# Kernel tuning notes

Measured on AMD Instinct MI355X. Metric: run time of the kernel, lower is better.

Reference implementation:

```python
import jax, jax.numpy as jnp
import numpy as np

N_HEAD, D_HEAD = 10, 38
D_MODEL, D_INNER = 380, 900
QLEN, BSZ = 1024, 4
MIN_LEN, MAX_LEN = -1024, 1024
EPS = 1e-5
SCALE = 1.0 / D_HEAD ** 0.5


def _ln(x, g, b):
    m = x.mean(-1, keepdims=True)
    v = ((x - m) ** 2).mean(-1, keepdims=True)
    return (x - m) / jnp.sqrt(v + EPS) * g + b


def setup_inputs() -> dict:
    key = jax.random.key(0)
    ks = jax.random.split(key, 10)
    s = 0.02
    w = jax.random.normal(ks[0], (QLEN, BSZ, D_MODEL), jnp.float32)
    # sinusoidal relative position embeddings over positions max_len .. min_len
    pos = jnp.arange(MAX_LEN, MIN_LEN - 1, -1, dtype=jnp.float32)  # [rlen]
    inv_freq = 1.0 / (10000.0 ** (jnp.arange(0, D_MODEL, 2, dtype=jnp.float32) / D_MODEL))
    sin_inp = pos[:, None] * inv_freq[None, :]
    r = jnp.concatenate([jnp.sin(sin_inp), jnp.cos(sin_inp)], axis=-1)  # [rlen, d_model]
    # causal mask, True = attend; layout [qlen, klen, bsz]
    attn_mask = jnp.broadcast_to(jnp.tril(jnp.ones((QLEN, QLEN), bool))[:, :, None], (QLEN, QLEN, BSZ))
    attn_relpos = jax.random.randint(ks[1], (BSZ, QLEN, QLEN), MIN_LEN, MAX_LEN + 1).astype(jnp.int32)
    return {
        'w': w,
        'r': r,
        'r_w_bias': s * jax.random.normal(ks[2], (N_HEAD, D_HEAD), jnp.float32),
        'r_r_bias': s * jax.random.normal(ks[3], (N_HEAD, D_HEAD), jnp.float32),
        'qkv_w': s * jax.random.normal(ks[4], (3 * N_HEAD * D_HEAD, D_MODEL), jnp.float32),
        'r_w': s * jax.random.normal(ks[5], (N_HEAD * D_HEAD, D_MODEL), jnp.float32),
        'o_w': s * jax.random.normal(ks[6], (D_MODEL, N_HEAD * D_HEAD), jnp.float32),
        'ln1_g': jnp.ones(D_MODEL, jnp.float32), 'ln1_b': jnp.zeros(D_MODEL, jnp.float32),
        'ff_w1': s * jax.random.normal(ks[7], (D_INNER, D_MODEL), jnp.float32),
        'ff_b1': jnp.zeros(D_INNER, jnp.float32),
        'ff_w2': s * jax.random.normal(ks[8], (D_MODEL, D_INNER), jnp.float32),
        'ff_b2': jnp.zeros(D_MODEL, jnp.float32),
        'ln2_g': jnp.ones(D_MODEL, jnp.float32), 'ln2_b': jnp.zeros(D_MODEL, jnp.float32),
        'attn_mask': attn_mask,
        'attn_relpos': attn_relpos,
        'min_len': MIN_LEN,
        'max_len': MAX_LEN,
    }


def reference(w, r, r_w_bias, r_r_bias, qkv_w, r_w, o_w, ln1_g, ln1_b,
              ff_w1, ff_b1, ff_w2, ff_b2, ln2_g, ln2_b,
              attn_mask, attn_relpos, min_len, max_len):
    qlen, bsz, _ = w.shape
    # qkv projection (no mems, post-lnorm)
    heads = jnp.einsum('ibm,hm->ibh', w, qkv_w)  # [q, b, 3*nh*dh]
    q, k, v = jnp.split(heads, 3, axis=-1)
    q = q.reshape(qlen, bsz, N_HEAD, D_HEAD)
    k = k.reshape(qlen, bsz, N_HEAD, D_HEAD)
    v = v.reshape(qlen, bsz, N_HEAD, D_HEAD)
    rk = (r @ r_w.T).reshape(-1, N_HEAD, D_HEAD)  # [rlen, nh, dh]
    # content score AC and position score BD (Transformer-XL)
    AC = jnp.einsum('ibnd,jbnd->ijbn', q + r_w_bias, k)   # [q, k, b, n]
    BD = jnp.einsum('ibnd,jnd->ijbn', q + r_r_bias, rk)   # [q, rlen, b, n]
    # gather-based relative position indexing (attn_relpos path)
    idx = (max_len - jnp.clip(attn_relpos, min_len, max_len)).transpose(1, 2, 0)  # [q, k, b]
    idx4 = jnp.broadcast_to(idx[..., None], idx.shape + (N_HEAD,))
    BD = jnp.take_along_axis(BD, idx4, axis=1)            # [q, k, b, n]
    score = (AC + BD) * SCALE
    score = jnp.where(attn_mask[:, :, :, None], score, -jnp.inf)
    prob = jax.nn.softmax(score, axis=1)
    vec = jnp.einsum('ijbn,jbnd->ibnd', prob, v).reshape(qlen, bsz, N_HEAD * D_HEAD)
    attn_out = vec @ o_w.T
    out = _ln(w + attn_out, ln1_g, ln1_b)
    # position-wise FF, post-lnorm
    core = jax.nn.relu(out @ ff_w1.T + ff_b1) @ ff_w2.T + ff_b2
    return _ln(out + core, ln2_g, ln2_b)
```

## Files before the change

kernel.cpp:

```cpp
#include <hip/hip_runtime.h>
#include <math.h>

#define QLEN 1024
#define BSZ 4
#define NH 10
#define DH 38
#define DM 380
#define DI 900
#define H3 1140
#define RLEN 2049
#define RLP 2112
#define SCALE 0.16222142113076254f
#define KS 2

typedef unsigned short ushortt;
typedef __attribute__((ext_vector_type(8))) short short8;
typedef __attribute__((ext_vector_type(4))) float float4v;

__device__ __forceinline__ float bf2f(ushortt u) {
    return __uint_as_float(((unsigned int)u) << 16);
}
__device__ __forceinline__ ushortt f2bf(float f) {
    unsigned int u = __float_as_uint(f);
    u += 0x7fffu + ((u >> 16) & 1u);
    return (ushortt)(u >> 16);
}

__global__ __launch_bounds__(256)
void convpad(const float* __restrict__ src, ushortt* __restrict__ dst,
             int R, int C, int Rp, int Cp) {
    const int total = Rp * Cp;
    for (int i = blockIdx.x * 256 + threadIdx.x; i < total; i += gridDim.x * 256) {
        int r = i / Cp, c = i - r * Cp;
        float v = (r < R && c < C) ? src[(size_t)r * C + c] : 0.f;
        dst[i] = f2bf(v);
    }
}

__global__ __launch_bounds__(256)
void init_pads(float* __restrict__ qwp, float* __restrict__ Kp, float* __restrict__ Vp,
               ushortt* __restrict__ vec) {
    const int i = blockIdx.x * 256 + threadIdx.x;
    if (i < BSZ * NH * 1024 * 2) {
        size_t idx = (size_t)(i >> 1) * 40 + 38 + (i & 1);
        qwp[idx] = 0.f; Kp[idx] = 0.f; Vp[idx] = 0.f;
    }
    if (i < 4096 * 4) {
        vec[(size_t)(i >> 2) * 384 + 380 + (i & 3)] = 0;
    }
}

template<int EPI>
__global__ __launch_bounds__(256)
void gemm_mfma(const ushortt* __restrict__ A, const ushortt* __restrict__ B,
               const float* __restrict__ bias, void* __restrict__ Cout,
               int M, int N, int Kpp, int ldc,
               const float* __restrict__ bias2, float* __restrict__ out2,
               float* __restrict__ out3, float* __restrict__ out4) {
    __shared__ __align__(16) ushortt As[128 * 32];
    __shared__ __align__(16) ushortt Bs[64 * 32];
    const int tid = threadIdx.x;
    const int wid = tid >> 6, lane = tid & 63;
    const int bRow = blockIdx.y * 128, bCol = blockIdx.x * 64;

    float4v acc[2][4];
    const float4v zz = {0.f, 0.f, 0.f, 0.f};
    #pragma unroll
    for (int m = 0; m < 2; ++m)
        #pragma unroll
        for (int n = 0; n < 4; ++n) acc[m][n] = zz;

    const int arow = tid >> 1, acol = (tid & 1) * 16;
    const int brow = tid >> 2, bcol = (tid & 3) * 8;
    const int fr = lane & 15, kg = lane >> 4;

    for (int k0 = 0; k0 < Kpp; k0 += 32) {
        const ushortt* ag = A + (size_t)(bRow + arow) * Kpp + k0 + acol;
        float4v a0 = *(const float4v*)ag;
        float4v a1 = *(const float4v*)(ag + 8);
        const ushortt* bg = B + (size_t)(bCol + brow) * Kpp + k0 + bcol;
        float4v b0 = *(const float4v*)bg;
        __syncthreads();
        *(float4v*)&As[arow * 32 + acol] = a0;
        *(float4v*)&As[arow * 32 + acol + 8] = a1;
        *(float4v*)&Bs[brow * 32 + bcol] = b0;
        __syncthreads();

        short8 bf[4];
        #pragma unroll
        for (int n = 0; n < 4; ++n)
            bf[n] = *(const short8*)&Bs[(n * 16 + fr) * 32 + kg * 8];
        #pragma unroll
        for (int m = 0; m < 2; ++m) {
            short8 af = *(const short8*)&As[(wid * 32 + m * 16 + fr) * 32 + kg * 8];
            #pragma unroll
            for (int n = 0; n < 4; ++n)
                acc[m][n] = __builtin_amdgcn_mfma_f32_16x16x32_bf16(af, bf[n], acc[m][n], 0, 0, 0);
        }
    }

    #pragma unroll
    for (int m = 0; m < 2; ++m)
        #pragma unroll
        for (int n = 0; n < 4; ++n)
            #pragma unroll
            for (int j = 0; j < 4; ++j) {
                const int row = bRow + wid * 32 + m * 16 + (lane >> 4) * 4 + j;
                const int col = bCol + n * 16 + (lane & 15);
                const float v = acc[m][n][j];
                if (EPI == 0) {
                    if (row < M && col < N) ((float*)Cout)[(size_t)row * ldc + col] = v;
                } else if (EPI == 3) {
                    if (row < M && col < 928) {
                        float h = (col < DI) ? fmaxf(v + bias[col], 0.f) : 0.f;
                        ((ushortt*)Cout)[(size_t)row * 928 + col] = f2bf(h);
                    }
                } else if (EPI == 4) {
                    if (row < M && col < N) ((float*)Cout)[(size_t)row * ldc + col] = v + bias[col];
                } else if (EPI == 5) {
                    if (col < H3) {
                        int part = col / 380;
                        int c = col - part * 380;
                        int nh = c / 38, d = c - nh * 38;
                        int q = row >> 2, b2 = row & 3;
                        size_t idx = (((size_t)b2 * NH + nh) * 1024 + q) * 40 + d;
                        if (part == 0) {
                            ((float*)Cout)[idx] = v + bias[c];
                            ((ushortt*)out2)[(((size_t)b2 * NH + nh) * 1024 + q) * 64 + d]
                                = f2bf(v + bias2[c]);
                        } else if (part == 1) out3[idx] = v;
                        else out4[idx] = v;
                    }
                } else {
                    if (row < RLEN && col < DM) {
                        int nh = col / 38, d = col - nh * 38;
                        ((ushortt*)Cout)[((size_t)nh * RLP + row) * 64 + d] = f2bf(v);
                    }
                }
            }
}

__global__ __launch_bounds__(256)
void bd_gemm(const ushortt* __restrict__ qr, const ushortt* __restrict__ rk,
             ushortt* __restrict__ BD, int bofs) {
    __shared__ __align__(16) ushortt As[64][72];
    __shared__ __align__(16) ushortt Bs[32][72];
    __shared__ __align__(16) ushortt Call[64 * 32 * 10];
    const int tid = threadIdx.x;
    const int wid = tid >> 6, lane = tid & 63;
    const int jt = blockIdx.x, qt = blockIdx.y, lb = blockIdx.z;
    const int j0 = jt * 32, q0 = qt * 64;
    const int fr = lane & 15, kg = lane >> 4;
    const int jcount = min(32, RLEN - j0);

    for (int n = 0; n < NH; ++n) {
        const ushortt* Ab = qr + (((size_t)(bofs + lb) * NH + n) * 1024 + q0) * 64;
        const ushortt* Bb = rk + ((size_t)n * RLP + j0) * 64;
        __syncthreads();
        {
            int rr = tid >> 2, cc = (tid & 3) * 16;
            *(float4v*)&As[rr][cc] = *(const float4v*)(Ab + (size_t)rr * 64 + cc);
            *(float4v*)&As[rr][cc + 8] = *(const float4v*)(Ab + (size_t)rr * 64 + cc + 8);
            int br = tid >> 3, bc = (tid & 7) * 8;
            *(float4v*)&Bs[br][bc] = *(const float4v*)(Bb + (size_t)br * 64 + bc);
        }
        __syncthreads();
        float4v acc[2] = {{0.f,0.f,0.f,0.f},{0.f,0.f,0.f,0.f}};
        #pragma unroll
        for (int ks = 0; ks < 64; ks += 32) {
            short8 af = *(const short8*)&As[wid * 16 + fr][ks + kg * 8];
            #pragma unroll
            for (int c = 0; c < 2; ++c) {
                short8 bfr = *(const short8*)&Bs[c * 16 + fr][ks + kg * 8];
                acc[c] = __builtin_amdgcn_mfma_f32_16x16x32_bf16(af, bfr, acc[c], 0, 0, 0);
            }
        }
        #pragma unroll
        for (int c = 0; c < 2; ++c)
            #pragma unroll
            for (int jj = 0; jj < 4; ++jj) {
                int rq = wid * 16 + (lane >> 4) * 4 + jj;
                int cj = c * 16 + (lane & 15);
                Call[(rq * 32 + cj) * 10 + n] = f2bf(acc[c][jj]);
            }
    }
    __syncthreads();
    const int rowdw = jcount * 5;
    const unsigned* Cdw = (const unsigned*)Call;
    unsigned* G = (unsigned*)BD;
    for (int idx = tid; idx < 64 * rowdw; idx += 256) {
        int rr = idx / rowdw, rem = idx - rr * rowdw;
        size_t gdw = ((((size_t)lb * 1024 + q0 + rr) * RLEN + j0) * 10) / 2 + rem;
        G[gdw] = Cdw[rr * 160 + rem];
    }
}

__global__ __launch_bounds__(256)
void attn4(const float* __restrict__ qwp, const float* __restrict__ Kp,
           const float* __restrict__ Vp, const ushortt* __restrict__ BD,
           const int* __restrict__ relpos,
           float* __restrict__ op, float2* __restrict__ ml, int b0, int nb) {
    const int bid = blockIdx.x;
    const int xcd = bid & 7, t = bid >> 3;
    const int gl = t / 20, member = t - gl * 20;
    const int G = gl * 8 + xcd;
    const int qc = 31 - G / nb;
    const int lbd = G - (31 - qc) * nb;
    const int n = member % NH, s = member / NH;
    const int qbase = qc * 32;
    const int b = b0 + lbd;
    const int tid = threadIdx.x;
    const int row = tid >> 3, kg = tid & 7;
    const int qi = qbase + row;
    const size_t bn = (size_t)b * NH + n;
    const size_t prow = ((size_t)s * (BSZ * NH) + bn) * 1024 + qi;

    const int ntchunk = (qbase + 95) >> 6;
    const int tbeg = s * 8;
    const int tend = min(tbeg + 8, ntchunk);
    if (tbeg >= tend) {
        if (kg == 0) ml[prow] = make_float2(-INFINITY, 0.f);
        return;
    }

    __shared__ __align__(16) float KtL[64 * 40];
    __shared__ __align__(16) float VtL[64 * 40];
    __shared__ float pL[32 * 66];

    const float* Kbase = Kp + bn * 1024 * 40;
    const float* Vbase = Vp + bn * 1024 * 40;

    float4v qw[10];
    {
        const float4v* src = (const float4v*)(qwp + (bn * 1024 + qi) * 40);
        #pragma unroll
        for (int i = 0; i < 10; ++i) qw[i] = src[i];
    }
    float o[5] = {0.f, 0.f, 0.f, 0.f, 0.f};
    float mrun = -INFINITY, lrun = 0.f;
    const int* rp = relpos + ((size_t)b * QLEN + qi) * QLEN;
    const ushortt* bdrow = BD + (((size_t)lbd * 1024 + qi) * RLEN) * NH + n;

    int jv[8]; float bdv[8];
    {
        const int k0 = tbeg * 64;
        #pragma unroll
        for (int ss = 0; ss < 8; ++ss) {
            const int kk = k0 + kg + ss * 8;
            int j = -1;
            if (kk <= qi) {
                int rpv = rp[kk];
                rpv = rpv < -1024 ? -1024 : (rpv > 1024 ? 1024 : rpv);
                j = 1024 - rpv;
            }
            jv[ss] = j;
        }
        #pragma unroll
        for (int ss = 0; ss < 8; ++ss)
            bdv[ss] = (jv[ss] >= 0) ? bf2f(bdrow[(size_t)jv[ss] * NH]) : 0.f;
    }

    for (int kt = tbeg; kt < tend; ++kt) {
        const int k0 = kt * 64;
        __syncthreads();
        {
            const float4v* ks = (const float4v*)(Kbase + (size_t)k0 * 40);
            const float4v* vs = (const float4v*)(Vbase + (size_t)k0 * 40);
            for (int e = tid; e < 640; e += 256) {
                ((float4v*)KtL)[e] = ks[e];
                ((float4v*)VtL)[e] = vs[e];
            }
        }
        __syncthreads();

        float sarr[8];
        float pmax = -INFINITY;
        #pragma unroll
        for (int ss = 0; ss < 8; ++ss) {
            float sv = -INFINITY;
            if (jv[ss] >= 0) {
                const int k = kg + ss * 8;
                float acc1 = 0.f;
                const float4v* kt4 = (const float4v*)(KtL + k * 40);
                #pragma unroll
                for (int i = 0; i < 10; ++i) {
                    float4v kv = kt4[i];
                    acc1 += qw[i][0] * kv[0] + qw[i][1] * kv[1]
                          + qw[i][2] * kv[2] + qw[i][3] * kv[3];
                }
                sv = (acc1 + bdv[ss]) * SCALE;
            }
            sarr[ss] = sv;
            pmax = fmaxf(pmax, sv);
        }
        pmax = fmaxf(pmax, __shfl_xor(pmax, 1, 64));
        pmax = fmaxf(pmax, __shfl_xor(pmax, 2, 64));
        pmax = fmaxf(pmax, __shfl_xor(pmax, 4, 64));
        const float nm = fmaxf(mrun, pmax);
        const float corr = __expf(mrun - nm);
        float psum = 0.f;
        float* prw = pL + row * 66;
        #pragma unroll
        for (int ss = 0; ss < 8; ++ss) {
            float p = __expf(sarr[ss] - nm);
            psum += p;
            prw[kg + ss * 8] = p;
        }
        psum += __shfl_xor(psum, 1, 64);
        psum += __shfl_xor(psum, 2, 64);
        psum += __shfl_xor(psum, 4, 64);
        lrun = lrun * corr + psum;
        mrun = nm;
        #pragma unroll
        for (int jj = 0; jj < 5; ++jj) o[jj] *= corr;

        int jn[8]; float bdn[8];
        if (kt + 1 < tend) {
            const int k0n = (kt + 1) * 64;
            #pragma unroll
            for (int ss = 0; ss < 8; ++ss) {
                const int kk = k0n + kg + ss * 8;
                int j = -1;
                if (kk <= qi) {
                    int rpv = rp[kk];
                    rpv = rpv < -1024 ? -1024 : (rpv > 1024 ? 1024 : rpv);
                    j = 1024 - rpv;
                }
                jn[ss] = j;
            }
            #pragma unroll
            for (int ss = 0; ss < 8; ++ss)
                bdn[ss] = (jn[ss] >= 0) ? bf2f(bdrow[(size_t)jn[ss] * NH]) : 0.f;
        } else {
            #pragma unroll
            for (int ss = 0; ss < 8; ++ss) { jn[ss] = -1; bdn[ss] = 0.f; }
        }

        int kmax = qi - k0 + 1; if (kmax > 64) kmax = 64;
        #pragma unroll 4
        for (int k = 0; k < kmax; ++k) {
            float p = prw[k];
            const float* vr = VtL + k * 40;
            float4v v4 = *(const float4v*)(vr + 4 * kg);
            float v1 = vr[32 + kg];
            o[0] += p * v4[0]; o[1] += p * v4[1];
            o[2] += p * v4[2]; o[3] += p * v4[3];
            o[4] += p * v1;
        }
        #pragma unroll
        for (int ss = 0; ss < 8; ++ss) { jv[ss] = jn[ss]; bdv[ss] = bdn[ss]; }
    }
    float* oprow = op + prow * 40;
    #pragma unroll
    for (int jj = 0; jj < 4; ++jj) oprow[4 * kg + jj] = o[jj];
    oprow[32 + kg] = o[4];
    if (kg == 0) ml[prow] = make_float2(mrun, lrun);
}

__global__ __launch_bounds__(256)
void attn_combine(const float* __restrict__ op, const float2* __restrict__ ml,
                  ushortt* __restrict__ vec) {
    const int idx = blockIdx.x * 256 + threadIdx.x;
    if (idx >= BSZ * NH * 1024 * 38) return;
    const int d = idx % 38;
    const int rh = idx / 38;
    const int q = rh & 1023;
    const int bn = rh >> 10;
    const int b = bn / NH, n = bn - b * NH;
    const float2 a = ml[rh];
    const float2 c = ml[(size_t)BSZ * NH * 1024 + rh];
    const float M = fmaxf(a.x, c.x);
    float l = 0.f, o = 0.f;
    if (a.y > 0.f) {
        float w = __expf(a.x - M);
        l += a.y * w;
        o += op[(size_t)rh * 40 + d] * w;
    }
    if (c.y > 0.f) {
        float w = __expf(c.x - M);
        l += c.y * w;
        o += op[((size_t)BSZ * NH * 1024 + rh) * 40 + d] * w;
    }
    vec[((size_t)q * BSZ + b) * 384 + (size_t)n * 38 + d] = f2bf(o / l);
}

template<bool WRITE_BF>
__global__ __launch_bounds__(256)
void ln_kernel(const float* __restrict__ x1, const float* __restrict__ x2,
               const float* __restrict__ g, const float* __restrict__ bb,
               float* __restrict__ outf, ushortt* __restrict__ outbf) {
    const int row = blockIdx.x;
    const float* p1 = x1 + (size_t)row * DM;
    const float* p2 = x2 + (size_t)row * DM;
    __shared__ float xb[DM];
    __shared__ float red[256];
    const int tid = threadIdx.x;
    float s = 0.f;
    for (int i = tid; i < DM; i += 256) { float v = p1[i] + p2[i]; xb[i] = v; s += v; }
    red[tid] = s; __syncthreads();
    for (int st = 128; st > 0; st >>= 1) { if (tid < st) red[tid] += red[tid + st]; __syncthreads(); }
    const float mean = red[0] / DM;
    __syncthreads();
    float s2 = 0.f;
    for (int i = tid; i < DM; i += 256) { float d = xb[i] - mean; s2 += d * d; }
    red[tid] = s2; __syncthreads();
    for (int st = 128; st > 0; st >>= 1) { if (tid < st) red[tid] += red[tid + st]; __syncthreads(); }
    const float rstd = rsqrtf(red[0] / DM + 1e-5f);
    for (int i = tid; i < (WRITE_BF ? 384 : DM); i += 256) {
        float v = 0.f;
        if (i < DM) {
            v = (xb[i] - mean) * rstd * g[i] + bb[i];
            outf[(size_t)row * DM + i] = v;
        }
        if (WRITE_BF) outbf[(size_t)row * 384 + i] = f2bf(i < DM ? v : 0.f);
    }
}

extern "C" void kernel_launch(void* const* d_in, const int* in_sizes, int n_in,
                              void* d_out, int out_size, void* d_ws, size_t ws_size,
                              hipStream_t stream) {
    const float* w     = (const float*)d_in[0];
    const float* r     = (const float*)d_in[1];
    const float* rwb   = (const float*)d_in[2];
    const float* rrb   = (const float*)d_in[3];
    const float* qkv_w = (const float*)d_in[4];
    const float* r_w   = (const float*)d_in[5];
    const float* o_w   = (const float*)d_in[6];
    const float* ln1g  = (const float*)d_in[7];
    const float* ln1b  = (const float*)d_in[8];
    const float* ffw1  = (const float*)d_in[9];
    const float* ffb1  = (const float*)d_in[10];
    const float* ffw2  = (const float*)d_in[11];
    const float* ffb2  = (const float*)d_in[12];
    const float* ln2g  = (const float*)d_in[13];
    const float* ln2b  = (const float*)d_in[14];
    const int*   relpos = (const int*)d_in[16];
    float* out = (float*)d_out;

    char* cur = (char*)d_ws;
    auto alloc = [&](size_t bytes) { char* p = cur; cur += (bytes + 255) & ~(size_t)255; return p; };
    ushortt* w_bf    = (ushortt*)alloc((size_t)4096 * 384 * 2);
    ushortt* qkv_bf  = (ushortt*)alloc((size_t)1152 * 384 * 2);
    ushortt* r_bf    = (ushortt*)alloc((size_t)2176 * 384 * 2);
    ushortt* rw_bf   = (ushortt*)alloc((size_t)384 * 384 * 2);
    ushortt* ow_bf   = (ushortt*)alloc((size_t)384 * 384 * 2);
    ushortt* f1_bf   = (ushortt*)alloc((size_t)960 * 384 * 2);
    ushortt* f2_bf   = (ushortt*)alloc((size_t)384 * 928 * 2);
    float*   qwp     = (float*)alloc((size_t)BSZ * NH * 1024 * 40 * 4);
    float*   Kpp     = (float*)alloc((size_t)BSZ * NH * 1024 * 40 * 4);
    float*   Vpp     = (float*)alloc((size_t)BSZ * NH * 1024 * 40 * 4);
    ushortt* qr_bf   = (ushortt*)alloc((size_t)BSZ * NH * 1024 * 64 * 2);
    ushortt* rk_bf   = (ushortt*)alloc((size_t)NH * RLP * 64 * 2);
    ushortt* vec_bf  = (ushortt*)alloc((size_t)4096 * 384 * 2);
    ushortt* out1_bf = (ushortt*)alloc((size_t)4096 * 384 * 2);
    ushortt* h1_bf   = (ushortt*)alloc((size_t)4096 * 928 * 2);
    float*   attnf   = (float*)alloc((size_t)4096 * DM * 4);
    float*   out1f   = (float*)alloc((size_t)4096 * DM * 4);
    float*   core    = (float*)alloc((size_t)4096 * DM * 4);

    float*  op_part = attnf;
    float2* ml_part = (float2*)(attnf + (size_t)KS * BSZ * NH * 1024 * 40);

    const size_t bd_b_bytes = (size_t)1024 * RLEN * NH * 2;
    ushortt* BD = (ushortt*)alloc(bd_b_bytes * BSZ);
    bool full = ((size_t)(cur - (char*)d_ws) <= ws_size);
    if (!full) { cur = (char*)BD; BD = (ushortt*)alloc(bd_b_bytes); }

    auto cgrid = [](size_t total) { return dim3((unsigned)((total + 255) / 256)); };
    hipMemsetAsync(qr_bf, 0, (size_t)BSZ * NH * 1024 * 64 * 2, stream);
    hipMemsetAsync(rk_bf, 0, (size_t)NH * RLP * 64 * 2, stream);
    convpad<<<cgrid((size_t)4096 * 384), 256, 0, stream>>>(w, w_bf, 4096, DM, 4096, 384);
    convpad<<<cgrid((size_t)1152 * 384), 256, 0, stream>>>(qkv_w, qkv_bf, H3, DM, 1152, 384);
    convpad<<<cgrid((size_t)2176 * 384), 256, 0, stream>>>(r, r_bf, RLEN, DM, 2176, 384);
    convpad<<<cgrid((size_t)384 * 384), 256, 0, stream>>>(r_w, rw_bf, DM, DM, 384, 384);
    convpad<<<cgrid((size_t)384 * 384), 256, 0, stream>>>(o_w, ow_bf, DM, DM, 384, 384);
    convpad<<<cgrid((size_t)960 * 384), 256, 0, stream>>>(ffw1, f1_bf, DI, DM, 960, 384);
    convpad<<<cgrid((size_t)384 * 928), 256, 0, stream>>>(ffw2, f2_bf, DM, DI, 384, 928);
    init_pads<<<cgrid((size_t)BSZ * NH * 1024 * 2), 256, 0, stream>>>(qwp, Kpp, Vpp, vec_bf);

    gemm_mfma<5><<<dim3(18, 32), 256, 0, stream>>>(w_bf, qkv_bf, rwb, qwp, 4096, H3, 384, 0,
                                                   rrb, (float*)qr_bf, Kpp, Vpp);
    gemm_mfma<6><<<dim3(6, 17), 256, 0, stream>>>(r_bf, rw_bf, nullptr, rk_bf, RLEN, DM, 384, 0,
                                                  nullptr, nullptr, nullptr, nullptr);
    if (full) {
        bd_gemm<<<dim3(65, 16, BSZ), 256, 0, stream>>>(qr_bf, rk_bf, BD, 0);
        attn4<<<dim3(2560), 256, 0, stream>>>(qwp, Kpp, Vpp, BD, relpos,
                                              op_part, ml_part, 0, BSZ);
    } else {
        for (int b = 0; b < BSZ; ++b) {
            bd_gemm<<<dim3(65, 16, 1), 256, 0, stream>>>(qr_bf, rk_bf, BD, b);
            attn4<<<dim3(640), 256, 0, stream>>>(qwp, Kpp, Vpp, BD, relpos,
                                                 op_part, ml_part, b, 1);
        }
    }
    attn_combine<<<cgrid((size_t)BSZ * NH * 1024 * 38), 256, 0, stream>>>(op_part, ml_part, vec_bf);
    gemm_mfma<0><<<dim3(6, 32), 256, 0, stream>>>(vec_bf, ow_bf, nullptr, attnf, 4096, DM, 384, DM,
                                                  nullptr, nullptr, nullptr, nullptr);
    ln_kernel<true><<<4096, 256, 0, stream>>>(w, attnf, ln1g, ln1b, out1f, out1_bf);
    gemm_mfma<3><<<dim3(15, 32), 256, 0, stream>>>(out1_bf, f1_bf, ffb1, h1_bf, 4096, DI, 384, 928,
                                                   nullptr, nullptr, nullptr, nullptr);
    gemm_mfma<4><<<dim3(6, 32), 256, 0, stream>>>(h1_bf, f2_bf, ffb2, core, 4096, DM, 928, DM,
                                                  nullptr, nullptr, nullptr, nullptr);
    ln_kernel<false><<<4096, 256, 0, stream>>>(out1f, core, ln2g, ln2b, out, nullptr);
}
```

Before: 405.9 us.

## Split attention key range into up to four chunks, store K/V and partials in bf16

The attention kernel now splits each query chunk's key range into chunks of four 64-key tiles, giving up to four splits instead of two. A new block-index mapping assigns blocks only to splits that have work, and the grid grows from 2560 to 3200 blocks. K and V are written by the QKV GEMM as bf16 and converted to fp32 when loaded into shared memory, which halves their global traffic. Partial outputs are also stored as bf16, and the combine kernel merges a variable number of splits. In exchange, the software prefetch of relpos/BD for the next tile is dropped, and bf16 K/V and partials lose some precision.

After: 402.4 us. About the same (-0.8%).

```diff
diff --git a/kernel.cpp b/kernel.cpp
--- a/kernel.cpp
+++ b/kernel.cpp
@@ -11,7 +11,6 @@
 #define RLEN 2049
 #define RLP 2112
 #define SCALE 0.16222142113076254f
-#define KS 2
 
 typedef unsigned short ushortt;
 typedef __attribute__((ext_vector_type(8))) short short8;
@@ -38,12 +37,12 @@
 }
 
 __global__ __launch_bounds__(256)
-void init_pads(float* __restrict__ qwp, float* __restrict__ Kp, float* __restrict__ Vp,
+void init_pads(float* __restrict__ qwp, ushortt* __restrict__ Kb, ushortt* __restrict__ Vb,
                ushortt* __restrict__ vec) {
     const int i = blockIdx.x * 256 + threadIdx.x;
     if (i < BSZ * NH * 1024 * 2) {
         size_t idx = (size_t)(i >> 1) * 40 + 38 + (i & 1);
-        qwp[idx] = 0.f; Kp[idx] = 0.f; Vp[idx] = 0.f;
+        qwp[idx] = 0.f; Kb[idx] = 0; Vb[idx] = 0;
     }
     if (i < 4096 * 4) {
         vec[(size_t)(i >> 2) * 384 + 380 + (i & 3)] = 0;
@@ -128,8 +127,8 @@
                             ((float*)Cout)[idx] = v + bias[c];
                             ((ushortt*)out2)[(((size_t)b2 * NH + nh) * 1024 + q) * 64 + d]
                                 = f2bf(v + bias2[c]);
-                        } else if (part == 1) out3[idx] = v;
-                        else out4[idx] = v;
+                        } else if (part == 1) ((ushortt*)out3)[idx] = f2bf(v);
+                        else ((ushortt*)out4)[idx] = f2bf(v);
                     }
                 } else {
                     if (row < RLEN && col < DM) {
@@ -196,39 +195,40 @@
 }
 
 __global__ __launch_bounds__(256)
-void attn4(const float* __restrict__ qwp, const float* __restrict__ Kp,
-           const float* __restrict__ Vp, const ushortt* __restrict__ BD,
+void attn5(const float* __restrict__ qwp, const ushortt* __restrict__ Kp,
+           const ushortt* __restrict__ Vp, const ushortt* __restrict__ BD,
            const int* __restrict__ relpos,
-           float* __restrict__ op, float2* __restrict__ ml, int b0, int nb) {
+           ushortt* __restrict__ op, float2* __restrict__ ml, int b0, int nb) {
     const int bid = blockIdx.x;
     const int xcd = bid & 7, t = bid >> 3;
-    const int gl = t / 20, member = t - gl * 20;
+    const int gl = t / 10, n = t - gl * 10;
     const int G = gl * 8 + xcd;
-    const int qc = 31 - G / nb;
-    const int lbd = G - (31 - qc) * nb;
-    const int n = member % NH, s = member / NH;
+    int qc, lb, s;
+    {
+        const int c3 = 32 * nb, c2 = 24 * nb, c1 = 16 * nb;
+        if (G < c3)                { qc = 31 - G / (4 * nb); int r2 = G % (4 * nb); lb = r2 >> 2; s = r2 & 3; }
+        else if (G < c3 + c2)      { int l2 = G - c3; qc = 23 - l2 / (3 * nb); int r2 = l2 % (3 * nb); lb = r2 / 3; s = r2 % 3; }
+        else if (G < c3 + c2 + c1) { int l2 = G - c3 - c2; qc = 15 - l2 / (2 * nb); int r2 = l2 % (2 * nb); lb = r2 >> 1; s = r2 & 1; }
+        else                       { int l2 = G - c3 - c2 - c1; qc = 7 - l2 / nb; lb = l2 % nb; s = 0; }
+    }
     const int qbase = qc * 32;
-    const int b = b0 + lbd;
+    const int b = b0 + lb;
     const int tid = threadIdx.x;
     const int row = tid >> 3, kg = tid & 7;
     const int qi = qbase + row;
     const size_t bn = (size_t)b * NH + n;
     const size_t prow = ((size_t)s * (BSZ * NH) + bn) * 1024 + qi;
 
-    const int ntchunk = (qbase + 95) >> 6;
-    const int tbeg = s * 8;
-    const int tend = min(tbeg + 8, ntchunk);
-    if (tbeg >= tend) {
-        if (kg == 0) ml[prow] = make_float2(-INFINITY, 0.f);
-        return;
-    }
+    const int ntiles = (qbase + 95) >> 6;
+    const int tbeg = s * 4;
+    const int tend = min(tbeg + 4, ntiles);
 
     __shared__ __align__(16) float KtL[64 * 40];
     __shared__ __align__(16) float VtL[64 * 40];
     __shared__ float pL[32 * 66];
 
-    const float* Kbase = Kp + bn * 1024 * 40;
-    const float* Vbase = Vp + bn * 1024 * 40;
+    const ushortt* Kbase = Kp + bn * 1024 * 40;
+    const ushortt* Vbase = Vp + bn * 1024 * 40;
 
     float4v qw[10];
     {
@@ -239,11 +239,29 @@
     float o[5] = {0.f, 0.f, 0.f, 0.f, 0.f};
     float mrun = -INFINITY, lrun = 0.f;
     const int* rp = relpos + ((size_t)b * QLEN + qi) * QLEN;
-    const ushortt* bdrow = BD + (((size_t)lbd * 1024 + qi) * RLEN) * NH + n;
-
-    int jv[8]; float bdv[8];
-    {
-        const int k0 = tbeg * 64;
+    const ushortt* bdrow = BD + (((size_t)lb * 1024 + qi) * RLEN) * NH + n;
+
+    for (int kt = tbeg; kt < tend; ++kt) {
+        const int k0 = kt * 64;
+        __syncthreads();
+        {
+            const short8* ks = (const short8*)(Kbase + (size_t)k0 * 40);
+            const short8* vs = (const short8*)(Vbase + (size_t)k0 * 40);
+            for (int e = tid; e < 320; e += 256) {
+                short8 kv = ks[e], vv = vs[e];
+                float4v k0v, k1v, v0v, v1v;
+                #pragma unroll
+                for (int x = 0; x < 4; ++x) {
+                    k0v[x] = bf2f((ushortt)kv[x]);     k1v[x] = bf2f((ushortt)kv[4 + x]);
+                    v0v[x] = bf2f((ushortt)vv[x]);     v1v[x] = bf2f((ushortt)vv[4 + x]);
+                }
+                ((float4v*)KtL)[e * 2] = k0v; ((float4v*)KtL)[e * 2 + 1] = k1v;
+                ((float4v*)VtL)[e * 2] = v0v; ((float4v*)VtL)[e * 2 + 1] = v1v;
+            }
+        }
+        __syncthreads();
+
+        int jv[8];
         #pragma unroll
         for (int ss = 0; ss < 8; ++ss) {
             const int kk = k0 + kg + ss * 8;
@@ -255,23 +273,10 @@
             }
             jv[ss] = j;
         }
+        float bdv[8];
         #pragma unroll
         for (int ss = 0; ss < 8; ++ss)
             bdv[ss] = (jv[ss] >= 0) ? bf2f(bdrow[(size_t)jv[ss] * NH]) : 0.f;
-    }
-
-    for (int kt = tbeg; kt < tend; ++kt) {
-        const int k0 = kt * 64;
-        __syncthreads();
-        {
-            const float4v* ks = (const float4v*)(Kbase + (size_t)k0 * 40);
-            const float4v* vs = (const float4v*)(Vbase + (size_t)k0 * 40);
-            for (int e = tid; e < 640; e += 256) {
-                ((float4v*)KtL)[e] = ks[e];
-                ((float4v*)VtL)[e] = vs[e];
-            }
-        }
-        __syncthreads();
 
         float sarr[8];
         float pmax = -INFINITY;
@@ -313,29 +318,6 @@
         mrun = nm;
         #pragma unroll
         for (int jj = 0; jj < 5; ++jj) o[jj] *= corr;
-
-        int jn[8]; float bdn[8];
-        if (kt + 1 < tend) {
-            const int k0n = (kt + 1) * 64;
-            #pragma unroll
-            for (int ss = 0; ss < 8; ++ss) {
-                const int kk = k0n + kg + ss * 8;
-                int j = -1;
-                if (kk <= qi) {
-                    int rpv = rp[kk];
-                    rpv = rpv < -1024 ? -1024 : (rpv > 1024 ? 1024 : rpv);
-                    j = 1024 - rpv;
-                }
-                jn[ss] = j;
-            }
-            #pragma unroll
-            for (int ss = 0; ss < 8; ++ss)
-                bdn[ss] = (jn[ss] >= 0) ? bf2f(bdrow[(size_t)jn[ss] * NH]) : 0.f;
-        } else {
-            #pragma unroll
-            for (int ss = 0; ss < 8; ++ss) { jn[ss] = -1; bdn[ss] = 0.f; }
-        }
-
         int kmax = qi - k0 + 1; if (kmax > 64) kmax = 64;
         #pragma unroll 4
         for (int k = 0; k < kmax; ++k) {
@@ -347,18 +329,16 @@
             o[2] += p * v4[2]; o[3] += p * v4[3];
             o[4] += p * v1;
         }
-        #pragma unroll
-        for (int ss = 0; ss < 8; ++ss) { jv[ss] = jn[ss]; bdv[ss] = bdn[ss]; }
-    }
-    float* oprow = op + prow * 40;
+    }
+    ushortt* oprow = op + prow * 40;
     #pragma unroll
-    for (int jj = 0; jj < 4; ++jj) oprow[4 * kg + jj] = o[jj];
-    oprow[32 + kg] = o[4];
+    for (int jj = 0; jj < 4; ++jj) oprow[4 * kg + jj] = f2bf(o[jj]);
+    oprow[32 + kg] = f2bf(o[4]);
     if (kg == 0) ml[prow] = make_float2(mrun, lrun);
 }
 
 __global__ __launch_bounds__(256)
-void attn_combine(const float* __restrict__ op, const float2* __restrict__ ml,
+void attn_combine(const ushortt* __restrict__ op, const float2* __restrict__ ml,
                   ushortt* __restrict__ vec) {
     const int idx = blockIdx.x * 256 + threadIdx.x;
     if (idx >= BSZ * NH * 1024 * 38) return;
@@ -367,19 +347,19 @@
     const int q = rh & 1023;
     const int bn = rh >> 10;
     const int b = bn / NH, n = bn - b * NH;
-    const float2 a = ml[rh];
-    const float2 c = ml[(size_t)BSZ * NH * 1024 + rh];
-    const float M = fmaxf(a.x, c.x);
+    const int ns = ((q >> 5) >> 3) + 1;
+    const size_t stride = (size_t)BSZ * NH * 1024;
+    float M = -INFINITY;
+    float2 mv[4];
+    for (int sp = 0; sp < ns; ++sp) {
+        mv[sp] = ml[sp * stride + rh];
+        M = fmaxf(M, mv[sp].x);
+    }
     float l = 0.f, o = 0.f;
-    if (a.y > 0.f) {
-        float w = __expf(a.x - M);
-        l += a.y * w;
-        o += op[(size_t)rh * 40 + d] * w;
-    }
-    if (c.y > 0.f) {
-        float w = __expf(c.x - M);
-        l += c.y * w;
-        o += op[((size_t)BSZ * NH * 1024 + rh) * 40 + d] * w;
+    for (int sp = 0; sp < ns; ++sp) {
+        float w = __expf(mv[sp].x - M);
+        l += mv[sp].y * w;
+        o += bf2f(op[(sp * stride + rh) * 40 + d]) * w;
     }
     vec[((size_t)q * BSZ + b) * 384 + (size_t)n * 38 + d] = f2bf(o / l);
 }
@@ -447,8 +427,8 @@
     ushortt* f1_bf   = (ushortt*)alloc((size_t)960 * 384 * 2);
     ushortt* f2_bf   = (ushortt*)alloc((size_t)384 * 928 * 2);
     float*   qwp     = (float*)alloc((size_t)BSZ * NH * 1024 * 40 * 4);
-    float*   Kpp     = (float*)alloc((size_t)BSZ * NH * 1024 * 40 * 4);
-    float*   Vpp     = (float*)alloc((size_t)BSZ * NH * 1024 * 40 * 4);
+    ushortt* K_bf    = (ushortt*)alloc((size_t)BSZ * NH * 1024 * 40 * 2);
+    ushortt* V_bf    = (ushortt*)alloc((size_t)BSZ * NH * 1024 * 40 * 2);
     ushortt* qr_bf   = (ushortt*)alloc((size_t)BSZ * NH * 1024 * 64 * 2);
     ushortt* rk_bf   = (ushortt*)alloc((size_t)NH * RLP * 64 * 2);
     ushortt* vec_bf  = (ushortt*)alloc((size_t)4096 * 384 * 2);
@@ -458,8 +438,8 @@
     float*   out1f   = (float*)alloc((size_t)4096 * DM * 4);
     float*   core    = (float*)alloc((size_t)4096 * DM * 4);
 
-    float*  op_part = attnf;
-    float2* ml_part = (float2*)(attnf + (size_t)KS * BSZ * NH * 1024 * 40);
+    ushortt* op_part = (ushortt*)attnf;
+    float2*  ml_part = (float2*)((char*)attnf + (size_t)4 * BSZ * NH * 1024 * 40 * 2);
 
     const size_t bd_b_bytes = (size_t)1024 * RLEN * NH * 2;
     ushortt* BD = (ushortt*)alloc(bd_b_bytes * BSZ);
@@ -476,20 +456,20 @@
     convpad<<<cgrid((size_t)384 * 384), 256, 0, stream>>>(o_w, ow_bf, DM, DM, 384, 384);
     convpad<<<cgrid((size_t)960 * 384), 256, 0, stream>>>(ffw1, f1_bf, DI, DM, 960, 384);
     convpad<<<cgrid((size_t)384 * 928), 256, 0, stream>>>(ffw2, f2_bf, DM, DI, 384, 928);
-    init_pads<<<cgrid((size_t)BSZ * NH * 1024 * 2), 256, 0, stream>>>(qwp, Kpp, Vpp, vec_bf);
+    init_pads<<<cgrid((size_t)BSZ * NH * 1024 * 2), 256, 0, stream>>>(qwp, K_bf, V_bf, vec_bf);
 
     gemm_mfma<5><<<dim3(18, 32), 256, 0, stream>>>(w_bf, qkv_bf, rwb, qwp, 4096, H3, 384, 0,
-                                                   rrb, (float*)qr_bf, Kpp, Vpp);
+                                                   rrb, (float*)qr_bf, (float*)K_bf, (float*)V_bf);
     gemm_mfma<6><<<dim3(6, 17), 256, 0, stream>>>(r_bf, rw_bf, nullptr, rk_bf, RLEN, DM, 384, 0,
                                                   nullptr, nullptr, nullptr, nullptr);
     if (full) {
         bd_gemm<<<dim3(65, 16, BSZ), 256, 0, stream>>>(qr_bf, rk_bf, BD, 0);
-        attn4<<<dim3(2560), 256, 0, stream>>>(qwp, Kpp, Vpp, BD, relpos,
+        attn5<<<dim3(3200), 256, 0, stream>>>(qwp, K_bf, V_bf, BD, relpos,
                                               op_part, ml_part, 0, BSZ);
     } else {
         for (int b = 0; b < BSZ; ++b) {
             bd_gemm<<<dim3(65, 16, 1), 256, 0, stream>>>(qr_bf, rk_bf, BD, b);
-            attn4<<<dim3(640), 256, 0, stream>>>(qwp, Kpp, Vpp, BD, relpos,
+            attn5<<<dim3(800), 256, 0, stream>>>(qwp, K_bf, V_bf, BD, relpos,
                                                  op_part, ml_part, b, 1);
         }
     }
```
